# Kernel tuning notes

Measured on AMD Instinct MI355X. Metric: run time of the kernel, lower is better.

## Reference

```python
import jax, jax.numpy as jnp
import numpy as np

N_BUCKET, EPB, EMBED, K, TAU = 64, 8, 1024, 2, 1.0
EPS_NORM, EPS_W = 1e-12, 1e-9

def _l2norm(x):
    n = jnp.linalg.norm(x, axis=-1, keepdims=True)
    return x / jnp.maximum(n, EPS_NORM)

def setup_inputs() -> dict:
    key = jax.random.key(0)
    k1, k2, k3 = jax.random.split(key, 3)
    h = jax.random.normal(k1, (8, 2048, EMBED), dtype=jnp.float32)
    op_id = jax.random.randint(k2, (8, 2048), 0, N_BUCKET, dtype=jnp.int64)
    expert_key = jax.random.normal(k3, (N_BUCKET, EPB, EMBED), dtype=jnp.float32) / np.sqrt(EMBED)
    return {"h": h, "op_id": op_id, "expert_key": expert_key}

def reference(h, op_id, expert_key):
    # h: (B,T,C), op_id: (B,T), expert_key: (n_bucket, epb, C)
    bucket = jnp.clip(op_id, 0, N_BUCKET - 1)          # (B,T)
    h_n = _l2norm(h)                                    # (B,T,C)
    keys = _l2norm(expert_key)                          # (nb,epb,C)
    keys_bt = keys[bucket]                              # gather -> (B,T,epb,C)
    score = jnp.einsum('btc,btec->bte', h_n, keys_bt)   # (B,T,epb)
    score = score / max(TAU, 1e-6)
    probs_local = jax.nn.softmax(score, axis=-1)        # (B,T,epb)
    topv, local = jax.lax.top_k(probs_local, K)         # (B,T,k) each
    w = topv / (jnp.sum(topv, axis=-1, keepdims=True) + EPS_W)
    gid = bucket[..., None] * EPB + local               # (B,T,k) global expert ids
    return (gid, w)
```

## Files before the change

### kernel.cpp

```cpp
#include <hip/hip_runtime.h>
#include <cmath>

#define EMBED   1024
#define EPB     8
#define NB      64
#define KTOP    2

__global__ void key_rnorm_kernel(const float* __restrict__ ek,
                                 float* __restrict__ rnorm, int nrows) {
    int wave = (int)((blockIdx.x * blockDim.x + threadIdx.x) >> 6);
    int lane = threadIdx.x & 63;
    if (wave >= nrows) return;
    const float4* row = (const float4*)(ek + (size_t)wave * EMBED);
    float s = 0.f;
#pragma unroll
    for (int c = 0; c < 4; ++c) {
        float4 v = row[c * 64 + lane];
        s += v.x * v.x + v.y * v.y + v.z * v.z + v.w * v.w;
    }
#pragma unroll
    for (int off = 32; off; off >>= 1) s += __shfl_xor(s, off, 64);
    if (lane == 0) rnorm[wave] = 1.0f / fmaxf(sqrtf(s), 1e-12f);
}

__global__ void router_kernel(const float* __restrict__ h,
                              const int*   __restrict__ op_id,
                              const float* __restrict__ ek,
                              const float* __restrict__ rk,
                              float* __restrict__ out_gid,
                              float* __restrict__ out_w,
                              int ntok) {
    int wave = (int)((blockIdx.x * blockDim.x + threadIdx.x) >> 6);
    int lane = threadIdx.x & 63;
    if (wave >= ntok) return;

    int b = op_id[wave];
    b = min(max(b, 0), NB - 1);

    const float4* hrow = (const float4*)(h + (size_t)wave * EMBED);
    float4 hv[4];
    float hh = 0.f;
#pragma unroll
    for (int c = 0; c < 4; ++c) {
        hv[c] = hrow[c * 64 + lane];
        hh += hv[c].x * hv[c].x + hv[c].y * hv[c].y +
              hv[c].z * hv[c].z + hv[c].w * hv[c].w;
    }

    const float4* kbase = (const float4*)(ek + (size_t)b * EPB * EMBED);
    float dot[EPB];
#pragma unroll
    for (int e = 0; e < EPB; ++e) {
        float d = 0.f;
#pragma unroll
        for (int c = 0; c < 4; ++c) {
            float4 kv = kbase[e * 256 + c * 64 + lane];
            d += hv[c].x * kv.x + hv[c].y * kv.y +
                 hv[c].z * kv.z + hv[c].w * kv.w;
        }
        dot[e] = d;
    }

#pragma unroll
    for (int off = 32; off; off >>= 1) {
        hh += __shfl_xor(hh, off, 64);
#pragma unroll
        for (int e = 0; e < EPB; ++e) dot[e] += __shfl_xor(dot[e], off, 64);
    }

    if (lane == 0) {
        float rh = 1.0f / fmaxf(sqrtf(hh), 1e-12f);
        float sc[EPB];
        float m = -1e30f;
#pragma unroll
        for (int e = 0; e < EPB; ++e) {
            sc[e] = dot[e] * rh * rk[b * EPB + e];
            m = fmaxf(m, sc[e]);
        }
        float ex[EPB];
        float Z = 0.f;
#pragma unroll
        for (int e = 0; e < EPB; ++e) { ex[e] = expf(sc[e] - m); Z += ex[e]; }

        int i1 = 0;
#pragma unroll
        for (int e = 1; e < EPB; ++e) if (ex[e] > ex[i1]) i1 = e;
        int i2 = (i1 == 0) ? 1 : 0;
#pragma unroll
        for (int e = 0; e < EPB; ++e)
            if (e != i1 && ex[e] > ex[i2]) i2 = e;

        float p1 = ex[i1] / Z;
        float p2 = ex[i2] / Z;
        float wsum = p1 + p2 + 1e-9f;

        out_gid[(size_t)wave * KTOP + 0] = (float)(b * EPB + i1);
        out_gid[(size_t)wave * KTOP + 1] = (float)(b * EPB + i2);
        out_w  [(size_t)wave * KTOP + 0] = p1 / wsum;
        out_w  [(size_t)wave * KTOP + 1] = p2 / wsum;
    }
}

extern "C" void kernel_launch(void* const* d_in, const int* in_sizes, int n_in,
                              void* d_out, int out_size, void* d_ws, size_t ws_size,
                              hipStream_t stream) {
    const float* h     = (const float*)d_in[0];
    const int*   op_id = (const int*)  d_in[1];
    const float* ek    = (const float*)d_in[2];

    int ntok = in_sizes[1];
    int nrows = NB * EPB;

    float* rk      = (float*)d_ws;
    float* out_gid = (float*)d_out;
    float* out_w   = out_gid + (size_t)ntok * KTOP;

    int blocks1 = (nrows * 64 + 255) / 256;
    key_rnorm_kernel<<<blocks1, 256, 0, stream>>>(ek, rk, nrows);

    int blocks2 = (ntok * 64 + 255) / 256;
    router_kernel<<<blocks2, 256, 0, stream>>>(h, op_id, ek, rk, out_gid, out_w, ntok);
}
```

Baseline: 114.3 us.

## Map eight tokens per wavefront with eight lanes per token

The router kernel now gives each token an 8-lane group instead of a whole 64-lane wavefront, so one wave handles eight tokens and the grid shrinks eightfold. Each lane issues more independent float4 loads (eight per chunk) for memory-level parallelism, and the cross-lane reduction drops from six shuffle stages to three. The cost is a per-lane access pattern strided across groups, which may hurt coalescing of h loads, plus higher register pressure from the 8-wide load buffers.

```diff
diff --git a/kernel.cpp b/kernel.cpp
--- a/kernel.cpp
+++ b/kernel.cpp
@@ -23,52 +23,64 @@
     if (lane == 0) rnorm[wave] = 1.0f / fmaxf(sqrtf(s), 1e-12f);
 }
 
-__global__ void router_kernel(const float* __restrict__ h,
-                              const int*   __restrict__ op_id,
-                              const float* __restrict__ ek,
-                              const float* __restrict__ rk,
-                              float* __restrict__ out_gid,
-                              float* __restrict__ out_w,
-                              int ntok) {
-    int wave = (int)((blockIdx.x * blockDim.x + threadIdx.x) >> 6);
-    int lane = threadIdx.x & 63;
-    if (wave >= ntok) return;
+__global__ __launch_bounds__(256) void router_kernel(
+        const float* __restrict__ h,
+        const int*   __restrict__ op_id,
+        const float* __restrict__ ek,
+        const float* __restrict__ rk,
+        float* __restrict__ out_gid,
+        float* __restrict__ out_w,
+        int ntok) {
+    int lane  = threadIdx.x & 63;
+    int waveB = threadIdx.x >> 6;
+    int g     = lane >> 3;
+    int s     = lane & 7;
+    int t     = (blockIdx.x * 4 + waveB) * 8 + g;
+    if (t >= ntok) return;
 
-    int b = op_id[wave];
+    int b = op_id[t];
     b = min(max(b, 0), NB - 1);
 
-    const float4* hrow = (const float4*)(h + (size_t)wave * EMBED);
-    float4 hv[4];
+    const float4* h4 = (const float4*)h  + (size_t)t * 256;
+    const float4* k4 = (const float4*)ek + (size_t)b * (EPB * 256);
+
+    float dot[EPB] = {0.f,0.f,0.f,0.f,0.f,0.f,0.f,0.f};
     float hh = 0.f;
+
 #pragma unroll
     for (int c = 0; c < 4; ++c) {
-        hv[c] = hrow[c * 64 + lane];
-        hh += hv[c].x * hv[c].x + hv[c].y * hv[c].y +
-              hv[c].z * hv[c].z + hv[c].w * hv[c].w;
-    }
+        float4 hv[8];
+#pragma unroll
+        for (int j = 0; j < 8; ++j)
+            hv[j] = h4[c * 64 + j * 8 + s];
+#pragma unroll
+        for (int j = 0; j < 8; ++j)
+            hh += hv[j].x * hv[j].x + hv[j].y * hv[j].y +
+                  hv[j].z * hv[j].z + hv[j].w * hv[j].w;
 
-    const float4* kbase = (const float4*)(ek + (size_t)b * EPB * EMBED);
-    float dot[EPB];
 #pragma unroll
-    for (int e = 0; e < EPB; ++e) {
-        float d = 0.f;
+        for (int e = 0; e < EPB; ++e) {
+            const float4* ke = k4 + e * 256 + c * 64 + s;
+            float4 kv[8];
 #pragma unroll
-        for (int c = 0; c < 4; ++c) {
-            float4 kv = kbase[e * 256 + c * 64 + lane];
-            d += hv[c].x * kv.x + hv[c].y * kv.y +
-                 hv[c].z * kv.z + hv[c].w * kv.w;
+            for (int j = 0; j < 8; ++j) kv[j] = ke[j * 8];
+            float d = dot[e];
+#pragma unroll
+            for (int j = 0; j < 8; ++j)
+                d += hv[j].x * kv[j].x + hv[j].y * kv[j].y +
+                     hv[j].z * kv[j].z + hv[j].w * kv[j].w;
+            dot[e] = d;
         }
-        dot[e] = d;
     }
 
 #pragma unroll
-    for (int off = 32; off; off >>= 1) {
+    for (int off = 1; off < 8; off <<= 1) {
         hh += __shfl_xor(hh, off, 64);
 #pragma unroll
         for (int e = 0; e < EPB; ++e) dot[e] += __shfl_xor(dot[e], off, 64);
     }
 
-    if (lane == 0) {
+    if (s == 0) {
         float rh = 1.0f / fmaxf(sqrtf(hh), 1e-12f);
         float sc[EPB];
         float m = -1e30f;
@@ -94,10 +106,10 @@
         float p2 = ex[i2] / Z;
         float wsum = p1 + p2 + 1e-9f;
 
-        out_gid[(size_t)wave * KTOP + 0] = (float)(b * EPB + i1);
-        out_gid[(size_t)wave * KTOP + 1] = (float)(b * EPB + i2);
-        out_w  [(size_t)wave * KTOP + 0] = p1 / wsum;
-        out_w  [(size_t)wave * KTOP + 1] = p2 / wsum;
+        out_gid[(size_t)t * KTOP + 0] = (float)(b * EPB + i1);
+        out_gid[(size_t)t * KTOP + 1] = (float)(b * EPB + i2);
+        out_w  [(size_t)t * KTOP + 0] = p1 / wsum;
+        out_w  [(size_t)t * KTOP + 1] = p2 / wsum;
     }
 }
 
@@ -108,7 +120,7 @@
     const int*   op_id = (const int*)  d_in[1];
     const float* ek    = (const float*)d_in[2];
 
-    int ntok = in_sizes[1];
+    int ntok  = in_sizes[1];
     int nrows = NB * EPB;
 
     float* rk      = (float*)d_ws;
@@ -118,6 +130,6 @@
     int blocks1 = (nrows * 64 + 255) / 256;
     key_rnorm_kernel<<<blocks1, 256, 0, stream>>>(ek, rk, nrows);
 
-    int blocks2 = (ntok * 64 + 255) / 256;
+    int blocks2 = (ntok + 31) / 32;
     router_kernel<<<blocks2, 256, 0, stream>>>(h, op_id, ek, rk, out_gid, out_w, ntok);
 }
```

Result: no change. 116.0 us (+1.5%).

## Bucket tokens by expert group and keep normalized keys resident in registers

Applied to the files above, without the earlier changes.

A new compaction kernel groups token indices by bucket using atomic counters. The router then launches a fixed grid of 8 blocks per bucket, and each wave keeps that bucket's 8 expert keys, pre-scaled by their inverse norms, in registers while it loops over its assigned tokens. This removes the per-token reload of the key rows from cache. In exchange it adds a kernel launch and atomic contention, reads h in a scattered order, uses heavy register pressure and a grid of only 512 blocks, and an unused no-op branch is left in the router.

```diff
diff --git a/kernel.cpp b/kernel.cpp
--- a/kernel.cpp
+++ b/kernel.cpp
@@ -7,7 +7,9 @@
 #define KTOP    2
 
 __global__ void key_rnorm_kernel(const float* __restrict__ ek,
-                                 float* __restrict__ rnorm, int nrows) {
+                                 float* __restrict__ rnorm,
+                                 int* __restrict__ cnt, int nrows) {
+    if (blockIdx.x == 0 && threadIdx.x < NB) cnt[threadIdx.x] = 0;
     int wave = (int)((blockIdx.x * blockDim.x + threadIdx.x) >> 6);
     int lane = threadIdx.x & 63;
     if (wave >= nrows) return;
@@ -23,81 +25,120 @@
     if (lane == 0) rnorm[wave] = 1.0f / fmaxf(sqrtf(s), 1e-12f);
 }
 
-__global__ void router_kernel(const float* __restrict__ h,
-                              const int*   __restrict__ op_id,
-                              const float* __restrict__ ek,
-                              const float* __restrict__ rk,
-                              float* __restrict__ out_gid,
-                              float* __restrict__ out_w,
-                              int ntok) {
-    int wave = (int)((blockIdx.x * blockDim.x + threadIdx.x) >> 6);
-    int lane = threadIdx.x & 63;
-    if (wave >= ntok) return;
+__global__ void compact_kernel(const int* __restrict__ op_id,
+                               int* __restrict__ cnt,
+                               int* __restrict__ list, int ntok) {
+    int t = blockIdx.x * blockDim.x + threadIdx.x;
+    if (t >= ntok) return;
+    int b = op_id[t];
+    b = min(max(b, 0), NB - 1);
+    int slot = atomicAdd(&cnt[b], 1);
+    list[(size_t)b * ntok + slot] = t;
+}
 
-    int b = op_id[wave];
-    b = min(max(b, 0), NB - 1);
+__global__ __launch_bounds__(256, 1) void router_kernel(
+        const float* __restrict__ h,
+        const float* __restrict__ ek,
+        const float* __restrict__ rk,
+        const int*   __restrict__ cnt,
+        const int*   __restrict__ list,
+        float* __restrict__ out_gid,
+        float* __restrict__ out_w,
+        int ntok) {
+    const int b    = blockIdx.x >> 3;
+    const int part = blockIdx.x & 7;
+    const int wv   = threadIdx.x >> 6;
+    const int lane = threadIdx.x & 63;
+    const int q    = part * 4 + wv;
 
-    const float4* hrow = (const float4*)(h + (size_t)wave * EMBED);
-    float4 hv[4];
-    float hh = 0.f;
+    const int n = cnt[b];
+    if (q * 1 >= n && q >= n) {  }
+    if (n == 0) return;
+
+    const float4* k4 = (const float4*)ek + (size_t)b * (EPB * 256);
+    float4 kv[EPB][4];
 #pragma unroll
-    for (int c = 0; c < 4; ++c) {
-        hv[c] = hrow[c * 64 + lane];
-        hh += hv[c].x * hv[c].x + hv[c].y * hv[c].y +
-              hv[c].z * hv[c].z + hv[c].w * hv[c].w;
-    }
+    for (int e = 0; e < EPB; ++e)
+#pragma unroll
+        for (int c = 0; c < 4; ++c)
+            kv[e][c] = k4[e * 256 + c * 64 + lane];
 
-    const float4* kbase = (const float4*)(ek + (size_t)b * EPB * EMBED);
-    float dot[EPB];
+    float rke[EPB];
 #pragma unroll
-    for (int e = 0; e < EPB; ++e) {
-        float d = 0.f;
+    for (int e = 0; e < EPB; ++e) rke[e] = rk[b * EPB + e];
+
+#pragma unroll
+    for (int e = 0; e < EPB; ++e)
 #pragma unroll
         for (int c = 0; c < 4; ++c) {
-            float4 kv = kbase[e * 256 + c * 64 + lane];
-            d += hv[c].x * kv.x + hv[c].y * kv.y +
-                 hv[c].z * kv.z + hv[c].w * kv.w;
+            kv[e][c].x *= rke[e]; kv[e][c].y *= rke[e];
+            kv[e][c].z *= rke[e]; kv[e][c].w *= rke[e];
         }
-        dot[e] = d;
-    }
+
+    const int* mylist = list + (size_t)b * ntok;
+
+    for (int i = q; i < n; i += 32) {
+        int t = mylist[i];
+        const float4* h4 = (const float4*)h + (size_t)t * 256;
+
+        float4 hv[4];
+        float hh = 0.f;
+#pragma unroll
+        for (int c = 0; c < 4; ++c) {
+            hv[c] = h4[c * 64 + lane];
+            hh += hv[c].x * hv[c].x + hv[c].y * hv[c].y +
+                  hv[c].z * hv[c].z + hv[c].w * hv[c].w;
+        }
+
+        float dot[EPB];
+#pragma unroll
+        for (int e = 0; e < EPB; ++e) {
+            float d = 0.f;
+#pragma unroll
+            for (int c = 0; c < 4; ++c)
+                d += hv[c].x * kv[e][c].x + hv[c].y * kv[e][c].y +
+                     hv[c].z * kv[e][c].z + hv[c].w * kv[e][c].w;
+            dot[e] = d;
+        }
 
 #pragma unroll
-    for (int off = 32; off; off >>= 1) {
-        hh += __shfl_xor(hh, off, 64);
+        for (int off = 32; off; off >>= 1) {
+            hh += __shfl_xor(hh, off, 64);
 #pragma unroll
-        for (int e = 0; e < EPB; ++e) dot[e] += __shfl_xor(dot[e], off, 64);
-    }
+            for (int e = 0; e < EPB; ++e) dot[e] += __shfl_xor(dot[e], off, 64);
+        }
 
-    if (lane == 0) {
-        float rh = 1.0f / fmaxf(sqrtf(hh), 1e-12f);
-        float sc[EPB];
-        float m = -1e30f;
+        if (lane == 0) {
+            float rh = 1.0f / fmaxf(sqrtf(hh), 1e-12f);
+            float sc[EPB];
+            float m = -1e30f;
 #pragma unroll
-        for (int e = 0; e < EPB; ++e) {
-            sc[e] = dot[e] * rh * rk[b * EPB + e];
-            m = fmaxf(m, sc[e]);
+            for (int e = 0; e < EPB; ++e) {
+                sc[e] = dot[e] * rh;
+                m = fmaxf(m, sc[e]);
+            }
+            float ex[EPB];
+            float Z = 0.f;
+#pragma unroll
+            for (int e = 0; e < EPB; ++e) { ex[e] = expf(sc[e] - m); Z += ex[e]; }
+
+            int i1 = 0;
+#pragma unroll
+            for (int e = 1; e < EPB; ++e) if (ex[e] > ex[i1]) i1 = e;
+            int i2 = (i1 == 0) ? 1 : 0;
+#pragma unroll
+            for (int e = 0; e < EPB; ++e)
+                if (e != i1 && ex[e] > ex[i2]) i2 = e;
+
+            float p1 = ex[i1] / Z;
+            float p2 = ex[i2] / Z;
+            float wsum = p1 + p2 + 1e-9f;
+
+            out_gid[(size_t)t * KTOP + 0] = (float)(b * EPB + i1);
+            out_gid[(size_t)t * KTOP + 1] = (float)(b * EPB + i2);
+            out_w  [(size_t)t * KTOP + 0] = p1 / wsum;
+            out_w  [(size_t)t * KTOP + 1] = p2 / wsum;
         }
-        float ex[EPB];
-        float Z = 0.f;
-#pragma unroll
-        for (int e = 0; e < EPB; ++e) { ex[e] = expf(sc[e] - m); Z += ex[e]; }
-
-        int i1 = 0;
-#pragma unroll
-        for (int e = 1; e < EPB; ++e) if (ex[e] > ex[i1]) i1 = e;
-        int i2 = (i1 == 0) ? 1 : 0;
-#pragma unroll
-        for (int e = 0; e < EPB; ++e)
-            if (e != i1 && ex[e] > ex[i2]) i2 = e;
-
-        float p1 = ex[i1] / Z;
-        float p2 = ex[i2] / Z;
-        float wsum = p1 + p2 + 1e-9f;
-
-        out_gid[(size_t)wave * KTOP + 0] = (float)(b * EPB + i1);
-        out_gid[(size_t)wave * KTOP + 1] = (float)(b * EPB + i2);
-        out_w  [(size_t)wave * KTOP + 0] = p1 / wsum;
-        out_w  [(size_t)wave * KTOP + 1] = p2 / wsum;
     }
 }
 
@@ -108,16 +149,21 @@
     const int*   op_id = (const int*)  d_in[1];
     const float* ek    = (const float*)d_in[2];
 
-    int ntok = in_sizes[1];
+    int ntok  = in_sizes[1];
     int nrows = NB * EPB;
 
-    float* rk      = (float*)d_ws;
+    float* rk   = (float*)d_ws;
+    int*   cnt  = (int*)(rk + 512);
+    int*   list = cnt + 64;
+
     float* out_gid = (float*)d_out;
     float* out_w   = out_gid + (size_t)ntok * KTOP;
 
     int blocks1 = (nrows * 64 + 255) / 256;
-    key_rnorm_kernel<<<blocks1, 256, 0, stream>>>(ek, rk, nrows);
+    key_rnorm_kernel<<<blocks1, 256, 0, stream>>>(ek, rk, cnt, nrows);
 
-    int blocks2 = (ntok * 64 + 255) / 256;
-    router_kernel<<<blocks2, 256, 0, stream>>>(h, op_id, ek, rk, out_gid, out_w, ntok);
+    compact_kernel<<<(ntok + 255) / 256, 256, 0, stream>>>(op_id, cnt, list, ntok);
+
+    router_kernel<<<NB * 8, 256, 0, stream>>>(h, ek, rk, cnt, list,
+                                              out_gid, out_w, ntok);
 }
```

Result: slower. 144.7 us (+26.5%).
